# Kernel optimization log

Hardware: AMD Instinct MI355X
Metric: run time of the kernel (lower is better)

## Reference

```python
import jax, jax.numpy as jnp
import numpy as np

EPS = 1e-05


def layer_norm(x, scale):
    # Faithful to source bug: returns scale * x_norm + scale (shift param unused)
    mean = jnp.mean(x, axis=-1, keepdims=True)
    var = jnp.var(x, axis=-1, keepdims=True)  # unbiased=False
    x_norm = (x - mean) / jnp.sqrt(var + EPS)
    return scale * x_norm + scale


def mhsa(x, wq, wk, wv, wo, bo, n_heads):
    b, t, d = x.shape
    hd = d // n_heads
    # torch Linear: y = x @ W.T (no qkv bias)
    q = (x @ wq.T).reshape(b, t, n_heads, hd).transpose(0, 2, 1, 3)  # bhtd
    k = (x @ wk.T).reshape(b, t, n_heads, hd).transpose(0, 2, 1, 3)
    v = (x @ wv.T).reshape(b, t, n_heads, hd).transpose(0, 2, 1, 3)
    scores = jnp.einsum('bhqd,bhkd->bhqk', q, k)
    causal = jnp.triu(jnp.ones((t, t), dtype=bool), k=1)
    scores = jnp.where(causal, -jnp.inf, scores)
    attn = jax.nn.softmax(scores / np.sqrt(hd).astype(np.float32), axis=-1)
    ctx = jnp.einsum('bhqk,bhkd->bhqd', attn, v)
    ctx = ctx.transpose(0, 2, 1, 3).reshape(b, t, d)
    return ctx @ wo.T + bo


def setup_inputs() -> dict:
    key = jax.random.key(0)
    ks = jax.random.split(key, 6)
    B, T, D = 2, 2048, 1024
    return {
        'x': jax.random.normal(ks[0], (B, T, D), dtype=jnp.float32),
        'wq': jax.random.normal(ks[1], (D, D), dtype=jnp.float32) * 0.02,
        'wk': jax.random.normal(ks[2], (D, D), dtype=jnp.float32) * 0.02,
        'wv': jax.random.normal(ks[3], (D, D), dtype=jnp.float32) * 0.02,
        'wo': jax.random.normal(ks[4], (D, D), dtype=jnp.float32) * 0.02,
        'bo': jnp.zeros((D,), dtype=jnp.float32),
        'ln1_scale': jnp.ones((D,), dtype=jnp.float32),
        'ln2_scale': jnp.ones((D,), dtype=jnp.float32),
    }


def reference(x, wq, wk, wv, wo, bo, ln1_scale, ln2_scale):
    n_heads = 16
    # Block 1: norm1 -> attn -> (+residual); dropout is identity in eval mode
    h = x + mhsa(layer_norm(x, ln1_scale), wq, wk, wv, wo, bo, n_heads)
    # Block 2: source calls self.attn (same weights) again, not self.ff
    out = h + mhsa(layer_norm(h, ln2_scale), wq, wk, wv, wo, bo, n_heads)
    return out
```

## Files before the change

kernel.cpp:

```cpp
#include <hip/hip_runtime.h>
#include <hip/hip_bf16.h>
#include <math.h>

#define Dm 1024
#define Tm 2048
#define Bm 2
#define Hm 16
#define HDm 64
#define Rm (Bm*Tm)
#define QKS 2048

typedef __attribute__((ext_vector_type(8))) short sh8;
typedef __attribute__((ext_vector_type(4))) float f32x4;
typedef __attribute__((ext_vector_type(16))) float f32x16;

#define AS1(p) ((const __attribute__((address_space(1))) void*)(p))
#define AS3(p) ((__attribute__((address_space(3))) void*)(p))

__device__ __forceinline__ short f2bs(float f) {
    union { float f; unsigned u; } v; v.f = f;
    unsigned r = v.u + 0x7FFFu + ((v.u >> 16) & 1u);
    return (short)(r >> 16);
}

__global__ __launch_bounds__(256) void convert_w(const float* __restrict__ wq,
                                                 const float* __restrict__ wk,
                                                 const float* __restrict__ wv,
                                                 const float* __restrict__ wo,
                                                 short* __restrict__ wqkv,
                                                 short* __restrict__ wob) {
    int idx = (blockIdx.x * 256 + threadIdx.x) * 4;
    const int M1 = 1 << 20;
    const float* src; short* dst; int off; float sc = 1.0f;
    if (idx < M1)           { src = wq; dst = wqkv;          off = idx; sc = 0.125f; }
    else if (idx < 2*M1)    { src = wk; dst = wqkv + M1;     off = idx - M1; }
    else if (idx < 3*M1)    { src = wv; dst = wqkv + 2*M1;   off = idx - 2*M1; }
    else                    { src = wo; dst = wob;           off = idx - 3*M1; }
    float4 v = *(const float4*)(src + off);
    short4 o;
    o.x = f2bs(v.x*sc); o.y = f2bs(v.y*sc); o.z = f2bs(v.z*sc); o.w = f2bs(v.w*sc);
    *(short4*)(dst + off) = o;
}

__global__ __launch_bounds__(256) void ln_kernel(const float* __restrict__ x,
                                                 const float* __restrict__ scale,
                                                 short* __restrict__ out) {
    int row = blockIdx.x;
    int t = threadIdx.x;
    const float4* xr = (const float4*)(x + (size_t)row * Dm);
    float4 v = xr[t];
    float s  = v.x + v.y + v.z + v.w;
    float ss = v.x*v.x + v.y*v.y + v.z*v.z + v.w*v.w;
    #pragma unroll
    for (int off = 32; off; off >>= 1) {
        s  += __shfl_xor(s, off);
        ss += __shfl_xor(ss, off);
    }
    __shared__ float red[8];
    int wave = t >> 6, lane = t & 63;
    if (lane == 0) { red[wave*2] = s; red[wave*2+1] = ss; }
    __syncthreads();
    s  = red[0] + red[2] + red[4] + red[6];
    ss = red[1] + red[3] + red[5] + red[7];
    float mean = s * (1.0f / Dm);
    float var  = ss * (1.0f / Dm) - mean * mean;
    float rstd = 1.0f / sqrtf(var + 1e-5f);
    float4 sc = ((const float4*)scale)[t];
    short4 o;
    o.x = f2bs(sc.x * ((v.x - mean) * rstd) + sc.x);
    o.y = f2bs(sc.y * ((v.y - mean) * rstd) + sc.y);
    o.z = f2bs(sc.z * ((v.z - mean) * rstd) + sc.z);
    o.w = f2bs(sc.w * ((v.w - mean) * rstd) + sc.w);
    ((short4*)(out + (size_t)row * Dm))[t] = o;
}

template<int BN, int MODE>
__global__ __launch_bounds__(256) void gemm_mfma(const short* __restrict__ A,
                                                 const short* __restrict__ B,
                                                 const float* __restrict__ bias,
                                                 const float* __restrict__ res,
                                                 void* __restrict__ Cv,
                                                 short* __restrict__ Vt,
                                                 int M, int N, int K) {
    __shared__ short As[128*32];
    __shared__ short Bs[BN*32];
    __shared__ short Tb[(MODE==1) ? 4*16*68 : 4];
    const int NJ = BN / 32;
    int t = threadIdx.x;
    int lane = t & 63, w = t >> 6;
    int l = lane & 15, quad = lane >> 4;
    int wm = (w & 1) * 64, wn = (w >> 1) * (BN/2);
    int m0 = blockIdx.y * 128, n0 = blockIdx.x * BN;

    f32x4 acc[4][NJ];
    #pragma unroll
    for (int i = 0; i < 4; i++)
        #pragma unroll
        for (int j = 0; j < NJ; j++)
            acc[i][j] = (f32x4){0.f,0.f,0.f,0.f};

    for (int k0 = 0; k0 < K; k0 += 32) {
        __syncthreads();
        #pragma unroll
        for (int p = 0; p < 2; p++) {
            int off = p*4096 + t*16;
            int row = off >> 6;
            int c = ((off >> 4) & 3) ^ (row & 3);
            const short* ga = A + (size_t)(m0 + row) * K + k0 + c*8;
            __builtin_amdgcn_global_load_lds(AS1(ga), AS3((char*)As + off), 16, 0, 0);
        }
        #pragma unroll
        for (int p = 0; p < BN/64; p++) {
            int off = p*4096 + t*16;
            int row = off >> 6;
            int c = ((off >> 4) & 3) ^ (row & 3);
            const short* gb = B + (size_t)(n0 + row) * K + k0 + c*8;
            __builtin_amdgcn_global_load_lds(AS1(gb), AS3((char*)Bs + off), 16, 0, 0);
        }
        __syncthreads();
        sh8 af[4], bf[NJ];
        #pragma unroll
        for (int i = 0; i < 4; i++) {
            int m = wm + i*16 + l;
            af[i] = *(const sh8*)((const char*)As + m*64 + ((quad ^ (m & 3)) * 16));
        }
        #pragma unroll
        for (int j = 0; j < NJ; j++) {
            int n = wn + j*16 + l;
            bf[j] = *(const sh8*)((const char*)Bs + n*64 + ((quad ^ (n & 3)) * 16));
        }
        #pragma unroll
        for (int i = 0; i < 4; i++)
            #pragma unroll
            for (int j = 0; j < NJ; j++)
                acc[i][j] = __builtin_amdgcn_mfma_f32_16x16x32_bf16(af[i], bf[j], acc[i][j], 0, 0, 0);
    }
    if (MODE == 0) {
        #pragma unroll
        for (int i = 0; i < 4; i++)
            #pragma unroll
            for (int j = 0; j < NJ; j++)
                #pragma unroll
                for (int r = 0; r < 4; r++) {
                    int m = m0 + wm + i*16 + quad*4 + r;
                    int n = n0 + wn + j*16 + l;
                    float vv = acc[i][j][r] + bias[n] + res[(size_t)m * N + n];
                    ((float*)Cv)[(size_t)m * N + n] = vv;
                }
    } else {
        if (n0 < 2048) {
            #pragma unroll
            for (int i = 0; i < 4; i++)
                #pragma unroll
                for (int j = 0; j < NJ; j++)
                    #pragma unroll
                    for (int r = 0; r < 4; r++) {
                        int m = m0 + wm + i*16 + quad*4 + r;
                        int n = n0 + wn + j*16 + l;
                        ((short*)Cv)[(size_t)m * QKS + n] = f2bs(acc[i][j][r]);
                    }
        } else {
            int bq = m0 >> 11;
            int key0 = (m0 & 2047) + wm;
            int h = (n0 + wn - 2048) >> 6;
            int quad2 = ((quad & 1) << 1) | (quad >> 1);
            short* vout = Vt + ((size_t)(bq*Hm + h) * HDm) * Tm + key0;
            #pragma unroll
            for (int j = 0; j < NJ; j++) {
                #pragma unroll
                for (int i = 0; i < 4; i++) {
                    short4 o;
                    o.x = f2bs(acc[i][j][0]); o.y = f2bs(acc[i][j][1]);
                    o.z = f2bs(acc[i][j][2]); o.w = f2bs(acc[i][j][3]);
                    *(short4*)&Tb[w*(16*68) + l*68 + i*16 + quad2*4] = o;
                }
                #pragma unroll
                for (int st = 0; st < 2; st++) {
                    int rr = st*8 + (lane >> 3);
                    int cc = lane & 7;
                    sh8 vv = *(const sh8*)&Tb[w*(16*68) + rr*68 + cc*8];
                    *(sh8*)(vout + (size_t)(j*16 + rr) * Tm + cc*8) = vv;
                }
            }
        }
    }
}

__global__ __launch_bounds__(128) void attn_mfma(const short* __restrict__ qk,
                                                 const short* __restrict__ vtg,
                                                 short* __restrict__ ctx) {
    __shared__ short Kl[3][64*64];
    __shared__ short Vl[2][64*64];
    int t = threadIdx.x;
    int lane = t & 63, w = t >> 6;
    int l31 = lane & 31, hi = lane >> 5;
    int bh = blockIdx.x;
    int xi = blockIdx.y;
    int cc0 = xi & 7, kk0 = xi >> 3;
    int qt = (kk0 == 0) ? cc0 : (kk0 == 1) ? (15 - cc0)
           : (kk0 == 2) ? (16 + cc0) : (31 - cc0);
    int b = bh >> 4, h = bh & 15;
    size_t rbase = (size_t)b * Tm;
    const short* qp0 = qk + rbase * QKS + h*HDm;
    const short* kp0 = qp0 + Dm;
    const short* vh  = vtg + ((size_t)bh * HDm) * Tm;
    int qtbase = qt * 64;
    int qrow = qtbase + w*32 + l31;

    sh8 qf[4];
    {
        const short* qp = qp0 + (size_t)qrow * QKS + hi*8;
        qf[0] = *(const sh8*)qp;
        qf[1] = *(const sh8*)(qp + 16);
        qf[2] = *(const sh8*)(qp + 32);
        qf[3] = *(const sh8*)(qp + 48);
    }

    f32x16 O0, O1;
    #pragma unroll
    for (int i = 0; i < 16; i++) { O0[i] = 0.f; O1[i] = 0.f; }
    float ps = 0.f;

    int trow = t >> 3;
    int c8 = ((t & 7) ^ (trow & 7)) * 8;
    int ldsoff = t * 16;
    const short* gkp = kp0 + (size_t)trow * QKS + c8;
    const short* gvp = vh + (size_t)trow * Tm + c8;

#define STAGE_K(KD) do { \
    __builtin_amdgcn_global_load_lds(AS1(gkp),                  AS3((char*)(KD) + ldsoff), 16, 0, 0); \
    __builtin_amdgcn_global_load_lds(AS1(gkp + (size_t)16*QKS), AS3((char*)(KD) + 2048 + ldsoff), 16, 0, 0); \
    __builtin_amdgcn_global_load_lds(AS1(gkp + (size_t)32*QKS), AS3((char*)(KD) + 4096 + ldsoff), 16, 0, 0); \
    __builtin_amdgcn_global_load_lds(AS1(gkp + (size_t)48*QKS), AS3((char*)(KD) + 6144 + ldsoff), 16, 0, 0); \
    gkp += (size_t)64*QKS; } while (0)

#define STAGE_V(VD) do { \
    __builtin_amdgcn_global_load_lds(AS1(gvp),                 AS3((char*)(VD) + ldsoff), 16, 0, 0); \
    __builtin_amdgcn_global_load_lds(AS1(gvp + (size_t)16*Tm), AS3((char*)(VD) + 2048 + ldsoff), 16, 0, 0); \
    __builtin_amdgcn_global_load_lds(AS1(gvp + (size_t)32*Tm), AS3((char*)(VD) + 4096 + ldsoff), 16, 0, 0); \
    __builtin_amdgcn_global_load_lds(AS1(gvp + (size_t)48*Tm), AS3((char*)(VD) + 6144 + ldsoff), 16, 0, 0); \
    gvp += 64; } while (0)

#define QKCOMP(KBUF) do { \
    const char* Kb_ = (const char*)(KBUF); \
    int sw_ = l31 & 7; \
    { const char* kr = Kb_ + l31*128; \
      f32x16 c; \
      _Pragma("unroll") for (int i_ = 0; i_ < 16; i_++) c[i_] = 0.f; \
      _Pragma("unroll") for (int s_ = 0; s_ < 4; s_++) { \
          sh8 kf = *(const sh8*)(kr + (((s_*2 + hi) ^ sw_) * 16)); \
          c = __builtin_amdgcn_mfma_f32_32x32x16_bf16(kf, qf[s_], c, 0, 0, 0); } \
      S0 = c; } \
    { const char* kr = Kb_ + (32 + l31)*128; \
      f32x16 c; \
      _Pragma("unroll") for (int i_ = 0; i_ < 16; i_++) c[i_] = 0.f; \
      _Pragma("unroll") for (int s_ = 0; s_ < 4; s_++) { \
          sh8 kf = *(const sh8*)(kr + (((s_*2 + hi) ^ sw_) * 16)); \
          c = __builtin_amdgcn_mfma_f32_32x32x16_bf16(kf, qf[s_], c, 0, 0, 0); } \
      S1 = c; } \
} while (0)

    STAGE_K(Kl[0]);
    STAGE_V(Vl[0]);
    if (qt >= 1) STAGE_K(Kl[1]);
    __syncthreads();

    f32x16 S0, S1;
    QKCOMP(Kl[0]);

    int bcur = 0;
    for (int kc = 0; kc <= qt; kc++) {
        int kbase = kc * 64;
        sh8 pa[4];
        {
            bool needmask = (kbase + 63 > qtbase + w*32);
            float p_[16];
            if (needmask) {
                #pragma unroll
                for (int r = 0; r < 16; r++) {
                    int key_r = kbase + (r&3) + 8*(r>>2) + 4*hi;
                    p_[r] = (key_r > qrow) ? 0.f : __expf(S0[r]);
                }
            } else {
                #pragma unroll
                for (int r = 0; r < 16; r++) p_[r] = __expf(S0[r]);
            }
            ps += (((p_[0]+p_[1])+(p_[2]+p_[3])) + ((p_[4]+p_[5])+(p_[6]+p_[7])))
                + (((p_[8]+p_[9])+(p_[10]+p_[11])) + ((p_[12]+p_[13])+(p_[14]+p_[15])));
            #pragma unroll
            for (int gg = 0; gg < 2; gg++) {
                union { __hip_bfloat162 h2[4]; sh8 s8; } u;
                u.h2[0] = __float22bfloat162_rn({p_[gg*8+0], p_[gg*8+1]});
                u.h2[1] = __float22bfloat162_rn({p_[gg*8+2], p_[gg*8+3]});
                u.h2[2] = __float22bfloat162_rn({p_[gg*8+4], p_[gg*8+5]});
                u.h2[3] = __float22bfloat162_rn({p_[gg*8+6], p_[gg*8+7]});
                pa[gg] = u.s8;
            }
            if (needmask) {
                #pragma unroll
                for (int r = 0; r < 16; r++) {
                    int key_r = kbase + 32 + (r&3) + 8*(r>>2) + 4*hi;
                    p_[r] = (key_r > qrow) ? 0.f : __expf(S1[r]);
                }
            } else {
                #pragma unroll
                for (int r = 0; r < 16; r++) p_[r] = __expf(S1[r]);
            }
            ps += (((p_[0]+p_[1])+(p_[2]+p_[3])) + ((p_[4]+p_[5])+(p_[6]+p_[7])))
                + (((p_[8]+p_[9])+(p_[10]+p_[11])) + ((p_[12]+p_[13])+(p_[14]+p_[15])));
            #pragma unroll
            for (int gg = 0; gg < 2; gg++) {
                union { __hip_bfloat162 h2[4]; sh8 s8; } u;
                u.h2[0] = __float22bfloat162_rn({p_[gg*8+0], p_[gg*8+1]});
                u.h2[1] = __float22bfloat162_rn({p_[gg*8+2], p_[gg*8+3]});
                u.h2[2] = __float22bfloat162_rn({p_[gg*8+4], p_[gg*8+5]});
                u.h2[3] = __float22bfloat162_rn({p_[gg*8+6], p_[gg*8+7]});
                pa[2 + gg] = u.s8;
            }
        }

        __syncthreads();

        int bnext = (bcur == 2) ? 0 : bcur + 1;
        if (kc + 2 <= qt) {
            int bnext2 = (bnext == 2) ? 0 : bnext + 1;
            STAGE_K(Kl[bnext2]);
        }
        if (kc + 1 <= qt) STAGE_V(Vl[(kc + 1) & 1]);

        if (kc < qt) QKCOMP(Kl[bnext]);

        const char* Vb = (const char*)Vl[kc & 1];
        {
            const char* vr = Vb + l31*128;
            int sw = l31 & 7;
            #pragma unroll
            for (int G = 0; G < 4; G++) {
                sh8 vf = *(const sh8*)(vr + (((G*2 + hi) ^ sw) * 16));
                O0 = __builtin_amdgcn_mfma_f32_32x32x16_bf16(pa[G], vf, O0, 0, 0, 0);
            }
        }
        {
            const char* vr = Vb + (32 + l31)*128;
            int sw = l31 & 7;
            #pragma unroll
            for (int G = 0; G < 4; G++) {
                sh8 vf = *(const sh8*)(vr + (((G*2 + hi) ^ sw) * 16));
                O1 = __builtin_amdgcn_mfma_f32_32x32x16_bf16(pa[G], vf, O1, 0, 0, 0);
            }
        }
        bcur = bnext;
    }
#undef STAGE_K
#undef STAGE_V
#undef QKCOMP

    ps += __shfl_xor(ps, 32);
    float inv_own = 1.0f / ps;
    short* cp = ctx + (rbase + qtbase + w*32) * Dm + h*HDm + l31;
    #pragma unroll
    for (int r = 0; r < 16; r++) {
        int rl = (r&3) + 8*(r>>2) + 4*hi;
        float inv = __shfl(inv_own, rl);
        cp[(size_t)rl * Dm]      = f2bs(O0[r] * inv);
        cp[(size_t)rl * Dm + 32] = f2bs(O1[r] * inv);
    }
}

extern "C" void kernel_launch(void* const* d_in, const int* in_sizes, int n_in,
                              void* d_out, int out_size, void* d_ws, size_t ws_size,
                              hipStream_t stream) {
    const float* x   = (const float*)d_in[0];
    const float* wq  = (const float*)d_in[1];
    const float* wk  = (const float*)d_in[2];
    const float* wv  = (const float*)d_in[3];
    const float* wo  = (const float*)d_in[4];
    const float* bo  = (const float*)d_in[5];
    const float* ln1 = (const float*)d_in[6];
    const float* ln2 = (const float*)d_in[7];
    float* out = (float*)d_out;

    short* lnb  = (short*)d_ws;
    short* ctxb = lnb  + (size_t)Rm*Dm;
    short* qk   = ctxb + (size_t)Rm*Dm;
    short* vtg  = qk   + (size_t)Rm*QKS;
    short* wqkv = vtg  + (size_t)Bm*Hm*HDm*Tm;
    short* wob  = wqkv + (size_t)3*Dm*Dm;

    dim3 qgrid(3072/128, Rm/128);
    dim3 pgrid(Dm/64,    Rm/128);
    dim3 agrid(32, 32);

    convert_w<<<4096, 256, 0, stream>>>(wq, wk, wv, wo, wqkv, wob);

    ln_kernel<<<Rm, 256, 0, stream>>>(x, ln1, lnb);
    gemm_mfma<128, 1><<<qgrid, 256, 0, stream>>>(lnb, wqkv, nullptr, nullptr, qk, vtg, Rm, 3072, Dm);
    attn_mfma<<<agrid, 128, 0, stream>>>(qk, vtg, ctxb);
    gemm_mfma<64, 0><<<pgrid, 256, 0, stream>>>(ctxb, wob, bo, x, out, nullptr, Rm, Dm, Dm);

    ln_kernel<<<Rm, 256, 0, stream>>>(out, ln2, lnb);
    gemm_mfma<128, 1><<<qgrid, 256, 0, stream>>>(lnb, wqkv, nullptr, nullptr, qk, vtg, Rm, 3072, Dm);
    attn_mfma<<<agrid, 128, 0, stream>>>(qk, vtg, ctxb);
    gemm_mfma<64, 0><<<pgrid, 256, 0, stream>>>(ctxb, wob, bo, out, out, nullptr, Rm, Dm, Dm);
}
```

Before: 301.1 us.

## Split attention key tile across four waves with LDS reduction of partial outputs

The attention kernel now uses 256 threads (4 waves) per block instead of 128. Each pair of waves handles one 32-key half of every 64-key tile, so each wave does half the QK^T, exp and PV work. Partial O accumulators and row sums from the second key-half are merged through LDS at the end. This doubles the waves available to hide latency and halves the per-wave serial chain, at the cost of an extra LDS reduction, barriers, and duplicated Q register loads.

```diff
diff --git a/kernel.cpp b/kernel.cpp
--- a/kernel.cpp
+++ b/kernel.cpp
@@ -186,13 +186,14 @@
     }
 }
 
-__global__ __launch_bounds__(128) void attn_mfma(const short* __restrict__ qk,
+__global__ __launch_bounds__(256) void attn_mfma(const short* __restrict__ qk,
                                                  const short* __restrict__ vtg,
                                                  short* __restrict__ ctx) {
     __shared__ short Kl[3][64*64];
     __shared__ short Vl[2][64*64];
     int t = threadIdx.x;
     int lane = t & 63, w = t >> 6;
+    int qh = w & 1, kh = w >> 1;
     int l31 = lane & 31, hi = lane >> 5;
     int bh = blockIdx.x;
     int xi = blockIdx.y;
@@ -205,7 +206,7 @@
     const short* kp0 = qp0 + Dm;
     const short* vh  = vtg + ((size_t)bh * HDm) * Tm;
     int qtbase = qt * 64;
-    int qrow = qtbase + w*32 + l31;
+    int qrow = qtbase + qh*32 + l31;
 
     sh8 qf[4];
     {
@@ -229,35 +230,23 @@
 
 #define STAGE_K(KD) do { \
     __builtin_amdgcn_global_load_lds(AS1(gkp),                  AS3((char*)(KD) + ldsoff), 16, 0, 0); \
-    __builtin_amdgcn_global_load_lds(AS1(gkp + (size_t)16*QKS), AS3((char*)(KD) + 2048 + ldsoff), 16, 0, 0); \
     __builtin_amdgcn_global_load_lds(AS1(gkp + (size_t)32*QKS), AS3((char*)(KD) + 4096 + ldsoff), 16, 0, 0); \
-    __builtin_amdgcn_global_load_lds(AS1(gkp + (size_t)48*QKS), AS3((char*)(KD) + 6144 + ldsoff), 16, 0, 0); \
     gkp += (size_t)64*QKS; } while (0)
 
 #define STAGE_V(VD) do { \
     __builtin_amdgcn_global_load_lds(AS1(gvp),                 AS3((char*)(VD) + ldsoff), 16, 0, 0); \
-    __builtin_amdgcn_global_load_lds(AS1(gvp + (size_t)16*Tm), AS3((char*)(VD) + 2048 + ldsoff), 16, 0, 0); \
     __builtin_amdgcn_global_load_lds(AS1(gvp + (size_t)32*Tm), AS3((char*)(VD) + 4096 + ldsoff), 16, 0, 0); \
-    __builtin_amdgcn_global_load_lds(AS1(gvp + (size_t)48*Tm), AS3((char*)(VD) + 6144 + ldsoff), 16, 0, 0); \
     gvp += 64; } while (0)
 
 #define QKCOMP(KBUF) do { \
-    const char* Kb_ = (const char*)(KBUF); \
+    const char* kr_ = (const char*)(KBUF) + (kh*32 + l31)*128; \
     int sw_ = l31 & 7; \
-    { const char* kr = Kb_ + l31*128; \
-      f32x16 c; \
-      _Pragma("unroll") for (int i_ = 0; i_ < 16; i_++) c[i_] = 0.f; \
-      _Pragma("unroll") for (int s_ = 0; s_ < 4; s_++) { \
-          sh8 kf = *(const sh8*)(kr + (((s_*2 + hi) ^ sw_) * 16)); \
-          c = __builtin_amdgcn_mfma_f32_32x32x16_bf16(kf, qf[s_], c, 0, 0, 0); } \
-      S0 = c; } \
-    { const char* kr = Kb_ + (32 + l31)*128; \
-      f32x16 c; \
-      _Pragma("unroll") for (int i_ = 0; i_ < 16; i_++) c[i_] = 0.f; \
-      _Pragma("unroll") for (int s_ = 0; s_ < 4; s_++) { \
-          sh8 kf = *(const sh8*)(kr + (((s_*2 + hi) ^ sw_) * 16)); \
-          c = __builtin_amdgcn_mfma_f32_32x32x16_bf16(kf, qf[s_], c, 0, 0, 0); } \
-      S1 = c; } \
+    f32x16 c_; \
+    _Pragma("unroll") for (int i_ = 0; i_ < 16; i_++) c_[i_] = 0.f; \
+    _Pragma("unroll") for (int s_ = 0; s_ < 4; s_++) { \
+        sh8 kf_ = *(const sh8*)(kr_ + (((s_*2 + hi) ^ sw_) * 16)); \
+        c_ = __builtin_amdgcn_mfma_f32_32x32x16_bf16(kf_, qf[s_], c_, 0, 0, 0); } \
+    S0 = c_; \
 } while (0)
 
     STAGE_K(Kl[0]);
@@ -265,20 +254,20 @@
     if (qt >= 1) STAGE_K(Kl[1]);
     __syncthreads();
 
-    f32x16 S0, S1;
+    f32x16 S0;
     QKCOMP(Kl[0]);
 
     int bcur = 0;
     for (int kc = 0; kc <= qt; kc++) {
         int kbase = kc * 64;
-        sh8 pa[4];
+        sh8 pa[2];
         {
-            bool needmask = (kbase + 63 > qtbase + w*32);
+            bool needmask = (kbase + kh*32 + 31 > qtbase + qh*32);
             float p_[16];
             if (needmask) {
                 #pragma unroll
                 for (int r = 0; r < 16; r++) {
-                    int key_r = kbase + (r&3) + 8*(r>>2) + 4*hi;
+                    int key_r = kbase + kh*32 + (r&3) + 8*(r>>2) + 4*hi;
                     p_[r] = (key_r > qrow) ? 0.f : __expf(S0[r]);
                 }
             } else {
@@ -296,27 +285,6 @@
                 u.h2[3] = __float22bfloat162_rn({p_[gg*8+6], p_[gg*8+7]});
                 pa[gg] = u.s8;
             }
-            if (needmask) {
-                #pragma unroll
-                for (int r = 0; r < 16; r++) {
-                    int key_r = kbase + 32 + (r&3) + 8*(r>>2) + 4*hi;
-                    p_[r] = (key_r > qrow) ? 0.f : __expf(S1[r]);
-                }
-            } else {
-                #pragma unroll
-                for (int r = 0; r < 16; r++) p_[r] = __expf(S1[r]);
-            }
-            ps += (((p_[0]+p_[1])+(p_[2]+p_[3])) + ((p_[4]+p_[5])+(p_[6]+p_[7])))
-                + (((p_[8]+p_[9])+(p_[10]+p_[11])) + ((p_[12]+p_[13])+(p_[14]+p_[15])));
-            #pragma unroll
-            for (int gg = 0; gg < 2; gg++) {
-                union { __hip_bfloat162 h2[4]; sh8 s8; } u;
-                u.h2[0] = __float22bfloat162_rn({p_[gg*8+0], p_[gg*8+1]});
-                u.h2[1] = __float22bfloat162_rn({p_[gg*8+2], p_[gg*8+3]});
-                u.h2[2] = __float22bfloat162_rn({p_[gg*8+4], p_[gg*8+5]});
-                u.h2[3] = __float22bfloat162_rn({p_[gg*8+6], p_[gg*8+7]});
-                pa[2 + gg] = u.s8;
-            }
         }
 
         __syncthreads();
@@ -331,23 +299,22 @@
         if (kc < qt) QKCOMP(Kl[bnext]);
 
         const char* Vb = (const char*)Vl[kc & 1];
+        int G0 = kh * 2;
         {
             const char* vr = Vb + l31*128;
             int sw = l31 & 7;
-            #pragma unroll
-            for (int G = 0; G < 4; G++) {
-                sh8 vf = *(const sh8*)(vr + (((G*2 + hi) ^ sw) * 16));
-                O0 = __builtin_amdgcn_mfma_f32_32x32x16_bf16(pa[G], vf, O0, 0, 0, 0);
-            }
+            sh8 v0 = *(const sh8*)(vr + ((((G0  )*2 + hi) ^ sw) * 16));
+            sh8 v1 = *(const sh8*)(vr + ((((G0+1)*2 + hi) ^ sw) * 16));
+            O0 = __builtin_amdgcn_mfma_f32_32x32x16_bf16(pa[0], v0, O0, 0, 0, 0);
+            O0 = __builtin_amdgcn_mfma_f32_32x32x16_bf16(pa[1], v1, O0, 0, 0, 0);
         }
         {
             const char* vr = Vb + (32 + l31)*128;
             int sw = l31 & 7;
-            #pragma unroll
-            for (int G = 0; G < 4; G++) {
-                sh8 vf = *(const sh8*)(vr + (((G*2 + hi) ^ sw) * 16));
-                O1 = __builtin_amdgcn_mfma_f32_32x32x16_bf16(pa[G], vf, O1, 0, 0, 0);
-            }
+            sh8 v0 = *(const sh8*)(vr + ((((G0  )*2 + hi) ^ sw) * 16));
+            sh8 v1 = *(const sh8*)(vr + ((((G0+1)*2 + hi) ^ sw) * 16));
+            O1 = __builtin_amdgcn_mfma_f32_32x32x16_bf16(pa[0], v0, O1, 0, 0, 0);
+            O1 = __builtin_amdgcn_mfma_f32_32x32x16_bf16(pa[1], v1, O1, 0, 0, 0);
         }
         bcur = bnext;
     }
@@ -356,14 +323,30 @@
 #undef QKCOMP
 
     ps += __shfl_xor(ps, 32);
-    float inv_own = 1.0f / ps;
-    short* cp = ctx + (rbase + qtbase + w*32) * Dm + h*HDm + l31;
-    #pragma unroll
-    for (int r = 0; r < 16; r++) {
-        int rl = (r&3) + 8*(r>>2) + 4*hi;
-        float inv = __shfl(inv_own, rl);
-        cp[(size_t)rl * Dm]      = f2bs(O0[r] * inv);
-        cp[(size_t)rl * Dm + 32] = f2bs(O1[r] * inv);
+    __syncthreads();
+    float* Lo  = (float*)Kl;
+    float* Lps = (float*)Vl;
+    if (kh == 1) {
+        #pragma unroll
+        for (int r = 0; r < 16; r++) {
+            int rl = (r&3) + 8*(r>>2) + 4*hi;
+            Lo[qh*2048 + rl*64 + l31]      = O0[r];
+            Lo[qh*2048 + rl*64 + 32 + l31] = O1[r];
+        }
+        if (hi == 0) Lps[qh*32 + l31] = ps;
+    }
+    __syncthreads();
+    if (kh == 0) {
+        float pst = ps + Lps[qh*32 + l31];
+        float inv_own = 1.0f / pst;
+        short* cp = ctx + (rbase + qtbase + qh*32) * Dm + h*HDm + l31;
+        #pragma unroll
+        for (int r = 0; r < 16; r++) {
+            int rl = (r&3) + 8*(r>>2) + 4*hi;
+            float inv = __shfl(inv_own, rl);
+            cp[(size_t)rl * Dm]      = f2bs((O0[r] + Lo[qh*2048 + rl*64 + l31]) * inv);
+            cp[(size_t)rl * Dm + 32] = f2bs((O1[r] + Lo[qh*2048 + rl*64 + 32 + l31]) * inv);
+        }
     }
 }
 
@@ -395,11 +378,11 @@
 
     ln_kernel<<<Rm, 256, 0, stream>>>(x, ln1, lnb);
     gemm_mfma<128, 1><<<qgrid, 256, 0, stream>>>(lnb, wqkv, nullptr, nullptr, qk, vtg, Rm, 3072, Dm);
-    attn_mfma<<<agrid, 128, 0, stream>>>(qk, vtg, ctxb);
+    attn_mfma<<<agrid, 256, 0, stream>>>(qk, vtg, ctxb);
     gemm_mfma<64, 0><<<pgrid, 256, 0, stream>>>(ctxb, wob, bo, x, out, nullptr, Rm, Dm, Dm);
 
     ln_kernel<<<Rm, 256, 0, stream>>>(out, ln2, lnb);
     gemm_mfma<128, 1><<<qgrid, 256, 0, stream>>>(lnb, wqkv, nullptr, nullptr, qk, vtg, Rm, 3072, Dm);
-    attn_mfma<<<agrid, 128, 0, stream>>>(qk, vtg, ctxb);
+    attn_mfma<<<agrid, 256, 0, stream>>>(qk, vtg, ctxb);
     gemm_mfma<64, 0><<<pgrid, 256, 0, stream>>>(ctxb, wob, bo, out, out, nullptr, Rm, Dm, Dm);
 }
```

Measured after the change: 284.6 us. 5.5% less time.
